# Optimization experiments

Hardware: AMD Instinct MI355X
Metric: run time of the kernel (lower is better)

The kernel has to match this reference:

```python
import jax, jax.numpy as jnp
import numpy as np

B, SQ, SC, DIM, H = 2, 2048, 2048, 1024, 16
HD = DIM // H  # 64
NEG = -10000.0


def setup_inputs() -> dict:
    key = jax.random.key(0)
    ks = jax.random.split(key, 12)
    x = jax.random.normal(ks[0], (B, SQ, DIM), dtype=jnp.float32)
    k_cache = jax.random.normal(ks[1], (B, SC, DIM), dtype=jnp.float32)
    v_cache = jax.random.normal(ks[2], (B, SC, DIM), dtype=jnp.float32)
    # binary additive-style mask (1 = masked), as multiplied by -10000 in forward
    mask = (jax.random.uniform(ks[3], (B, SQ, SQ + SC)) > 0.9).astype(jnp.float32)
    s = 1.0 / np.sqrt(DIM)
    Wq = jax.random.normal(ks[4], (DIM, DIM), dtype=jnp.float32) * s
    Wk = jax.random.normal(ks[5], (DIM, DIM), dtype=jnp.float32) * s
    Wv = jax.random.normal(ks[6], (DIM, DIM), dtype=jnp.float32) * s
    Wo = jax.random.normal(ks[7], (DIM, DIM), dtype=jnp.float32) * s
    bq = jnp.zeros((DIM,), jnp.float32)
    bk = jnp.zeros((DIM,), jnp.float32)
    bv = jnp.zeros((DIM,), jnp.float32)
    bo = jnp.zeros((DIM,), jnp.float32)
    return {"x": x, "k_cache": k_cache, "v_cache": v_cache, "mask": mask,
            "Wq": Wq, "bq": bq, "Wk": Wk, "bk": bk, "Wv": Wv, "bv": bv,
            "Wo": Wo, "bo": bo}


def reference(x, k_cache, v_cache, mask, Wq, bq, Wk, bk, Wv, bv, Wo, bo):
    # QKV projections (dropout is inference no-op)
    q = x @ Wq + bq                      # [B, SQ, DIM]
    k = jnp.concatenate([k_cache, x @ Wk + bk], axis=-2)  # [B, SKV, DIM]
    v = jnp.concatenate([v_cache, x @ Wv + bv], axis=-2)  # [B, SKV, DIM]
    skv = k.shape[-2]
    # split heads
    qh = q.reshape(B, SQ, H, HD).transpose(0, 2, 1, 3)    # [B, H, SQ, HD]
    kh = k.reshape(B, skv, H, HD).transpose(0, 2, 1, 3)   # [B, H, SKV, HD]
    vh = v.reshape(B, skv, H, HD).transpose(0, 2, 1, 3)   # [B, H, SKV, HD]
    scores = jnp.einsum('bhqd,bhkd->bhqk', qh, kh) / np.sqrt(HD)
    scores = scores + mask[:, None, :, :] * NEG           # additive mask
    attn = jax.nn.softmax(scores, axis=-1)
    ctx = jnp.einsum('bhqk,bhkd->bhqd', attn, vh)         # [B, H, SQ, HD]
    ctx = ctx.transpose(0, 2, 1, 3).reshape(B, SQ, DIM)
    out = ctx @ Wo + bo
    return (out, k, v)
```

## Files before the change

kernel.cpp:

```cpp
#include <hip/hip_runtime.h>
#include <hip/hip_bf16.h>

#define SQL  2048
#define SKVL 4096
#define DIML 1024

typedef __attribute__((ext_vector_type(8))) short short8;
typedef __attribute__((ext_vector_type(4))) float f32x4;

#define LOG2E 1.4426950408889634f
#define MBIGC (10000.0f * LOG2E)

#define GLL16(gptr, lptr)                                        \
  __builtin_amdgcn_global_load_lds(                              \
      (const __attribute__((address_space(1))) int*)(gptr),      \
      (__attribute__((address_space(3))) int*)(lptr), 16, 0, 0)

__device__ __forceinline__ short f2s(float f) {
  return __builtin_bit_cast(short, __float2bfloat16(f));
}
__device__ __forceinline__ float s2f(short s) {
  return __bfloat162float(__builtin_bit_cast(__hip_bfloat16, s));
}

__device__ __forceinline__ const char* swz_addr(const char* base, int row, int colByte) {
  return base + (row * 128 + (colByte ^ ((row & 7) << 4)));
}
__device__ __forceinline__ char* swz_addr(char* base, int row, int colByte) {
  return base + (row * 128 + (colByte ^ ((row & 7) << 4)));
}

__global__ __launch_bounds__(256) void prep_kernel(
    const float* __restrict__ x, short* __restrict__ xbf,
    const float* __restrict__ W0, const float* __restrict__ W1,
    const float* __restrict__ W2, const float* __restrict__ W3,
    short* __restrict__ WT,
    const float* __restrict__ kc, const float* __restrict__ vc,
    float* __restrict__ out, short* __restrict__ Kbf,
    const float* __restrict__ mask, unsigned long long* __restrict__ maskQ)
{
  __shared__ float T[64][65];
  const int bid = blockIdx.x;
  const int t = threadIdx.x;

  if (bid < 2048) {
    const size_t i = ((size_t)bid * 256 + t) * 8;
    float4 a = *(const float4*)&x[i];
    float4 b = *(const float4*)&x[i + 4];
    short8 o;
    o[0] = f2s(a.x); o[1] = f2s(a.y); o[2] = f2s(a.z); o[3] = f2s(a.w);
    o[4] = f2s(b.x); o[5] = f2s(b.y); o[6] = f2s(b.z); o[7] = f2s(b.w);
    *(short8*)&xbf[i] = o;
  } else if (bid < 3072) {
    const int lb = bid - 2048;
    const int w = lb >> 8;
    const float* W = (w == 0) ? W0 : (w == 1) ? W1 : (w == 2) ? W2 : W3;
    short* D = WT + (size_t)w * 1048576;
    const int tile = lb & 255;
    const int r0 = (tile >> 4) * 64;
    const int c0 = (tile & 15) * 64;
    const int row = t >> 2;
    const int q = t & 3;
#pragma unroll
    for (int i = 0; i < 4; i++)
      *(float4*)&T[row][q * 16 + i * 4] =
          *(const float4*)&W[(size_t)(r0 + row) * 1024 + c0 + q * 16 + i * 4];
    __syncthreads();
    short8 o0, o1;
#pragma unroll
    for (int j = 0; j < 8; j++) {
      o0[j] = f2s(T[q * 16 + j][row]);
      o1[j] = f2s(T[q * 16 + 8 + j][row]);
    }
    *(short8*)&D[(size_t)(c0 + row) * 1024 + r0 + q * 16] = o0;
    *(short8*)&D[(size_t)(c0 + row) * 1024 + r0 + q * 16 + 8] = o1;
  } else if (bid < 7168) {
    const int idx = (bid - 3072) * 256 + t;
    const int tensor = idx >> 19;
    const int cc = idx & 524287;
    const size_t e = (size_t)cc * 8;
    const int b = (int)(e >> 21);
    const size_t rem = e & 2097151;
    const float* src = tensor ? vc : kc;
    float* dst = out + (tensor ? 12582912u : 4194304u) + (size_t)b * 4194304u + rem;
    float4 a = *(const float4*)&src[e];
    float4 bb = *(const float4*)&src[e + 4];
    *(float4*)dst = a;
    *(float4*)(dst + 4) = bb;
    if (tensor == 0) {
      short8 o;
      o[0] = f2s(a.x); o[1] = f2s(a.y); o[2] = f2s(a.z); o[3] = f2s(a.w);
      o[4] = f2s(bb.x); o[5] = f2s(bb.y); o[6] = f2s(bb.z); o[7] = f2s(bb.w);
      *(short8*)&Kbf[(size_t)b * 4194304u + rem] = o;
    }
  } else {
    const int lb = bid - 7168;
    const int ktile = lb & 63;
    const int qtile = (lb >> 6) & 31;
    const int b = lb >> 11;
    const int q0 = qtile * 64, k0 = ktile * 64;
    const int row = t >> 2;
    const int q4 = t & 3;
    const float* src = mask + (size_t)(b * SQL + q0 + row) * SKVL + k0 + q4 * 16;
#pragma unroll
    for (int i = 0; i < 4; i++)
      *(float4*)&T[row][q4 * 16 + i * 4] = *(const float4*)&src[i * 4];
    __syncthreads();
    const int wv = t >> 6, ln = t & 63;
#pragma unroll
    for (int j = 0; j < 16; j++) {
      const int qrow = wv * 16 + j;
      unsigned long long w = __ballot(T[qrow][ln] > 0.5f);
      if (ln == 0)
        maskQ[(size_t)(b * SQL + q0 + qrow) * 64 + ktile] = w;
    }
  }
}

__global__ __launch_bounds__(256) void gemm_qkv(
    const short* __restrict__ A,
    const short* __restrict__ WT,
    const float* __restrict__ bq, const float* __restrict__ bk, const float* __restrict__ bv,
    short* __restrict__ qbf,
    float* __restrict__ kout, short* __restrict__ Kbf,
    float* __restrict__ vout, float qscale)
{
  constexpr int K = 1024;
  __shared__ __align__(16) short As[128 * 32];
  __shared__ __align__(16) short Bs[128 * 32];
  const int w = blockIdx.x >> 8;
  const int bid = blockIdx.x & 255;
  const int tid = threadIdx.x;
  const int lane = tid & 63;
  const int wave = tid >> 6;
  const int nb = bid & 7;
  const int mb = bid >> 3;
  const int wm = wave >> 1;
  const int wn = wave & 1;
  const int g = lane >> 4;
  const int fr = lane & 15;

  const short* BT = WT + (size_t)w * 1048576;
  const float* bias = (w == 0) ? bq : (w == 1) ? bk : bv;

  f32x4 acc[4][4] = {};

  const int c0 = tid, c1 = tid + 256;
  const short* Ab0 = A + (size_t)(mb * 128 + (c0 >> 2)) * K + (c0 & 3) * 8;
  const short* Ab1 = A + (size_t)(mb * 128 + (c1 >> 2)) * K + (c1 & 3) * 8;
  const short* Bb0 = BT + (size_t)(nb * 128 + (c0 >> 2)) * K + (c0 & 3) * 8;
  const short* Bb1 = BT + (size_t)(nb * 128 + (c1 >> 2)) * K + (c1 & 3) * 8;

  for (int k0 = 0; k0 < K; k0 += 32) {
    __syncthreads();
    GLL16(Ab0 + k0, &As[wave * 512]);
    GLL16(Ab1 + k0, &As[2048 + wave * 512]);
    GLL16(Bb0 + k0, &Bs[wave * 512]);
    GLL16(Bb1 + k0, &Bs[2048 + wave * 512]);
    __syncthreads();
    short8 af[4], bfv[4];
#pragma unroll
    for (int m = 0; m < 4; m++)
      af[m] = *(const short8*)&As[(wm * 64 + m * 16 + fr) * 32 + g * 8];
#pragma unroll
    for (int n = 0; n < 4; n++)
      bfv[n] = *(const short8*)&Bs[(wn * 64 + n * 16 + fr) * 32 + g * 8];
#pragma unroll
    for (int m = 0; m < 4; m++)
#pragma unroll
      for (int n = 0; n < 4; n++)
        acc[m][n] = __builtin_amdgcn_mfma_f32_16x16x32_bf16(af[m], bfv[n], acc[m][n], 0, 0, 0);
  }

  const int gm = mb * 128 + wm * 64;
  const int gn = nb * 128 + wn * 64;
  float bvv[4];
#pragma unroll
  for (int n = 0; n < 4; n++) bvv[n] = bias[gn + n * 16 + fr];
#pragma unroll
  for (int m = 0; m < 4; m++) {
#pragma unroll
    for (int r = 0; r < 4; r++) {
      const int row = gm + m * 16 + g * 4 + r;
      float vals[4];
      if (w == 0) {
#pragma unroll
        for (int n = 0; n < 4; n++) vals[n] = (acc[m][n][r] + bvv[n]) * qscale;
        const int drow = (row >> 11) * 2048 + (row & 2047);
#pragma unroll
        for (int n = 0; n < 4; n++)
          qbf[(size_t)drow * 1024 + gn + n * 16 + fr] = f2s(vals[n]);
      } else {
#pragma unroll
        for (int n = 0; n < 4; n++) vals[n] = acc[m][n][r] + bvv[n];
        const int drow = (row >> 11) * 4096 + 2048 + (row & 2047);
        if (w == 1) {
#pragma unroll
          for (int n = 0; n < 4; n++) {
            kout[(size_t)drow * 1024 + gn + n * 16 + fr] = vals[n];
            Kbf[(size_t)drow * 1024 + gn + n * 16 + fr] = f2s(vals[n]);
          }
        } else {
#pragma unroll
          for (int n = 0; n < 4; n++)
            vout[(size_t)drow * 1024 + gn + n * 16 + fr] = vals[n];
        }
      }
    }
  }
}

__global__ __launch_bounds__(256) void gemm_wo(
    const short* __restrict__ A,
    const short* __restrict__ BT,
    const float* __restrict__ bias,
    float* __restrict__ Cf)
{
  constexpr int K = 1024;
  __shared__ __align__(16) short As[128 * 32];
  __shared__ __align__(16) short Bs[64 * 32];
  const int tid = threadIdx.x;
  const int lane = tid & 63;
  const int wave = tid >> 6;
  const int bid = blockIdx.x;
  const int nb = bid & 15;
  const int mb = bid >> 4;
  const int wm = wave >> 1;
  const int wn = wave & 1;
  const int g = lane >> 4;
  const int fr = lane & 15;

  f32x4 acc[4][2] = {};

  const int c0 = tid, c1 = tid + 256;
  const short* Ab0 = A + (size_t)(mb * 128 + (c0 >> 2)) * K + (c0 & 3) * 8;
  const short* Ab1 = A + (size_t)(mb * 128 + (c1 >> 2)) * K + (c1 & 3) * 8;
  const short* Bb0 = BT + (size_t)(nb * 64 + (c0 >> 2)) * K + (c0 & 3) * 8;

  for (int k0 = 0; k0 < K; k0 += 32) {
    __syncthreads();
    GLL16(Ab0 + k0, &As[wave * 512]);
    GLL16(Ab1 + k0, &As[2048 + wave * 512]);
    GLL16(Bb0 + k0, &Bs[wave * 512]);
    __syncthreads();
    short8 af[4], bfv[2];
#pragma unroll
    for (int m = 0; m < 4; m++)
      af[m] = *(const short8*)&As[(wm * 64 + m * 16 + fr) * 32 + g * 8];
#pragma unroll
    for (int n = 0; n < 2; n++)
      bfv[n] = *(const short8*)&Bs[(wn * 32 + n * 16 + fr) * 32 + g * 8];
#pragma unroll
    for (int m = 0; m < 4; m++)
#pragma unroll
      for (int n = 0; n < 2; n++)
        acc[m][n] = __builtin_amdgcn_mfma_f32_16x16x32_bf16(af[m], bfv[n], acc[m][n], 0, 0, 0);
  }

  const int gm = mb * 128 + wm * 64;
  const int gn = nb * 64 + wn * 32;
  float bv[2];
#pragma unroll
  for (int n = 0; n < 2; n++) bv[n] = bias[gn + n * 16 + fr];
#pragma unroll
  for (int m = 0; m < 4; m++) {
#pragma unroll
    for (int r = 0; r < 4; r++) {
      const int row = gm + m * 16 + g * 4 + r;
#pragma unroll
      for (int n = 0; n < 2; n++)
        Cf[(size_t)row * 1024 + gn + n * 16 + fr] = acc[m][n][r] + bv[n];
    }
  }
}

__global__ __launch_bounds__(256) void transpose_v_kernel(
    const float* __restrict__ Vf, short* __restrict__ VT)
{
  __shared__ float T[64][65];
  const int bid = blockIdx.x;
  const int kb = bid & 63;
  const int h = (bid >> 6) & 15;
  const int b = bid >> 10;
  const int kt = kb * 64;
  const int t = threadIdx.x;
  const int row = t >> 2;
  const int q = t & 3;
  const float* src = Vf + (size_t)(b * SKVL + kt + row) * DIML + h * 64 + q * 16;
#pragma unroll
  for (int i = 0; i < 4; i++)
    *(float4*)&T[row][q * 16 + i * 4] = *(const float4*)&src[i * 4];
  __syncthreads();
  short8 o0, o1;
#pragma unroll
  for (int j = 0; j < 8; j++) {
    o0[j] = f2s(T[q * 16 + j][row]);
    o1[j] = f2s(T[q * 16 + 8 + j][row]);
  }
  short* D = VT + (size_t)((b * 16 + h) * 64 + row) * SKVL + kt;
  *(short8*)&D[q * 16] = o0;
  *(short8*)&D[q * 16 + 8] = o1;
}

__global__ __launch_bounds__(512) void attn_kernel(
    const short* __restrict__ Q,
    const short* __restrict__ Kb_,
    const short* __restrict__ VT_,
    const unsigned long long* __restrict__ maskQ,
    short* __restrict__ pctx,
    float2* __restrict__ ml)
{
  __shared__ __align__(16) char LDSB[32768];
  const int tid = threadIdx.x;
  const int lane = tid & 63;
  const int wave = tid >> 6;
  const int gid = blockIdx.x;
  const int xcd = gid & 7;
  const int seq = gid >> 3;
  const int group = xcd * 8 + (seq >> 4);
  const int qbB = seq & 15;
  const int half = group & 1;
  const int bh = group >> 1;
  const int b = bh >> 4;
  const int h = bh & 15;
  const int g = lane >> 4;
  const int c = lane & 15;

  const int qbase = qbB * 128 + wave * 16;

  short8 qf[2];
  {
    const short* qp = Q + (size_t)(b * SQL + qbase + c) * DIML + h * 64 + g * 8;
    qf[0] = *(const short8*)qp;
    qf[1] = *(const short8*)(qp + 32);
  }

  short8 vone;
#pragma unroll
  for (int j = 0; j < 8; j++) vone[j] = (short)0x3F80;

  float m_run = -1e30f;
  f32x4 ctx[4] = {};
  f32x4 lacc = {};

  const unsigned X = (unsigned)((c & 7) << 4);
  unsigned kA  = (unsigned)(c * 128) + (((unsigned)(g * 16)) ^ X);
  unsigned vA  = 8192u + (unsigned)(c * 128) + (((unsigned)(g * 16)) ^ X);
  unsigned pw0 = 16384u + (unsigned)(wave * 2048 + c * 128) +
                 (((unsigned)(g * 8)) ^ (X & 0x10u)) + (X & 0x60u);
  unsigned pr0 = 16384u + (unsigned)(wave * 2048 + c * 128) +
                 (((unsigned)(g * 16)) ^ X);
  asm volatile("" : "+v"(kA), "+v"(vA), "+v"(pw0), "+v"(pr0));

  const int k_beg = half * (SKVL / 2);
  const int srow = lane >> 3;
  const int scol = ((lane & 7) ^ srow) * 8;
  const short* gk = Kb_ + (size_t)b * SKVL * DIML + h * 64 +
                    (size_t)(k_beg + wave * 8 + srow) * DIML + scol;
  const short* gv = VT_ + (size_t)(b * 16 + h) * 64 * SKVL +
                    (size_t)(wave * 8 + srow) * SKVL + k_beg + scol;
  const unsigned long long* mqp =
      maskQ + (size_t)(b * SQL + qbase + c) * 64 + half * 32;
  const unsigned kdst = (unsigned)(wave * 8 * 128);
  const unsigned vdst = 8192u + (unsigned)(wave * 8 * 128);

  for (int t = 0; t < (SKVL / 2) / 64; t++) {
    if (t) __syncthreads();
    GLL16(gk, &LDSB[kdst]);
    GLL16(gv, &LDSB[vdst]);
    gk += 64 * DIML;
    gv += 64;
    const unsigned long long mq = *mqp++;

    __syncthreads();

    f32x4 s[4] = {};
#pragma unroll
    for (int n = 0; n < 4; n++) {
      short8 kf0 = *(const short8*)&LDSB[kA + (unsigned)(n * 2048)];
      short8 kf1 = *(const short8*)&LDSB[(kA ^ 64u) + (unsigned)(n * 2048)];
      s[n] = __builtin_amdgcn_mfma_f32_16x16x32_bf16(kf0, qf[0], s[n], 0, 0, 0);
      s[n] = __builtin_amdgcn_mfma_f32_16x16x32_bf16(kf1, qf[1], s[n], 0, 0, 0);
    }
#pragma unroll
    for (int n = 0; n < 4; n++) {
      const unsigned wn = (unsigned)(mq >> (n * 16 + g * 4)) & 0xFu;
#pragma unroll
      for (int r = 0; r < 4; r++)
        if ((wn >> r) & 1u) s[n][r] -= MBIGC;
    }
    float mx0 = fmaxf(fmaxf(s[0][0], s[0][1]), fmaxf(s[0][2], s[0][3]));
    float mx1 = fmaxf(fmaxf(s[1][0], s[1][1]), fmaxf(s[1][2], s[1][3]));
    float mx2 = fmaxf(fmaxf(s[2][0], s[2][1]), fmaxf(s[2][2], s[2][3]));
    float mx3 = fmaxf(fmaxf(s[3][0], s[3][1]), fmaxf(s[3][2], s[3][3]));
    const float mloc = fmaxf(fmaxf(mx0, mx1), fmaxf(mx2, mx3));
    if (__any(mloc > m_run + 11.5f)) {
      float mt = fmaxf(mloc, __shfl_xor(mloc, 16));
      mt = fmaxf(mt, __shfl_xor(mt, 32));
      const float mnew = fmaxf(m_run, mt);
      const float sc = exp2f(m_run - mnew);
      m_run = mnew;
#pragma unroll
      for (int r = 0; r < 4; r++) {
        const float scr = __shfl(sc, g * 4 + r);
        lacc[r] *= scr;
        ctx[0][r] *= scr; ctx[1][r] *= scr; ctx[2][r] *= scr; ctx[3][r] *= scr;
      }
    }
#pragma unroll
    for (int n = 0; n < 4; n++) {
      const float p0 = exp2f(s[n][0] - m_run);
      const float p1 = exp2f(s[n][1] - m_run);
      const float p2 = exp2f(s[n][2] - m_run);
      const float p3 = exp2f(s[n][3] - m_run);
      unsigned lo, hi;
      asm("v_cvt_pk_bf16_f32 %0, %1, %2" : "=v"(lo) : "v"(p0), "v"(p1));
      asm("v_cvt_pk_bf16_f32 %0, %1, %2" : "=v"(hi) : "v"(p2), "v"(p3));
      *(uint2*)&LDSB[pw0 ^ (unsigned)(n * 32)] = make_uint2(lo, hi);
    }
#pragma unroll
    for (int ks = 0; ks < 2; ks++) {
      short8 pa = *(const short8*)&LDSB[pr0 ^ (unsigned)(ks * 64)];
      lacc = __builtin_amdgcn_mfma_f32_16x16x32_bf16(pa, vone, lacc, 0, 0, 0);
#pragma unroll
      for (int d = 0; d < 4; d++) {
        short8 vfr = *(const short8*)&LDSB[(vA ^ (unsigned)(ks * 64)) + (unsigned)(d * 2048)];
        ctx[d] = __builtin_amdgcn_mfma_f32_16x16x32_bf16(pa, vfr, ctx[d], 0, 0, 0);
      }
    }
  }

#pragma unroll
  for (int r = 0; r < 4; r++) {
    const int rg = ((b * 16 + h) << 11) + qbase + g * 4 + r;
    const size_t base = ((size_t)half << 22) + (size_t)rg * 64;
#pragma unroll
    for (int d = 0; d < 4; d++)
      pctx[base + d * 16 + c] = f2s(ctx[d][r]);
    const float m_q = __shfl(m_run, g * 4 + r);
    if (c == 0) ml[half * 65536 + rg] = make_float2(m_q, lacc[r]);
  }
}

__global__ __launch_bounds__(256) void combine_kernel(
    const short* __restrict__ pctx, const float2* __restrict__ ml,
    short* __restrict__ ctxb)
{
  const int t = blockIdx.x * 256 + threadIdx.x;
  const int r = t >> 2;
  const int seg = (t & 3) * 16;
  const float2 ml0 = ml[r];
  const float2 ml1 = ml[65536 + r];
  const float m = fmaxf(ml0.x, ml1.x);
  const float w0 = exp2f(ml0.x - m);
  const float w1 = exp2f(ml1.x - m);
  const float inv = 1.0f / (ml0.y * w0 + ml1.y * w1);
  const short8 a0 = *(const short8*)&pctx[(size_t)r * 64 + seg];
  const short8 a1 = *(const short8*)&pctx[(size_t)r * 64 + seg + 8];
  const short8 b0 = *(const short8*)&pctx[(1ull << 22) + (size_t)r * 64 + seg];
  const short8 b1 = *(const short8*)&pctx[(1ull << 22) + (size_t)r * 64 + seg + 8];
  short8 o0, o1;
#pragma unroll
  for (int j = 0; j < 8; j++) {
    o0[j] = f2s((s2f(a0[j]) * w0 + s2f(b0[j]) * w1) * inv);
    o1[j] = f2s((s2f(a1[j]) * w0 + s2f(b1[j]) * w1) * inv);
  }
  const int b = r >> 15;
  const int h = (r >> 11) & 15;
  const int q = r & 2047;
  short* D = ctxb + (size_t)(b * 2048 + q) * 1024 + h * 64 + seg;
  *(short8*)&D[0] = o0;
  *(short8*)&D[8] = o1;
}

extern "C" void kernel_launch(void* const* d_in, const int* in_sizes, int n_in,
                              void* d_out, int out_size, void* d_ws, size_t ws_size,
                              hipStream_t stream)
{
  const float* x   = (const float*)d_in[0];
  const float* kc  = (const float*)d_in[1];
  const float* vc  = (const float*)d_in[2];
  const float* msk = (const float*)d_in[3];
  const float* Wq  = (const float*)d_in[4];
  const float* bq  = (const float*)d_in[5];
  const float* Wk  = (const float*)d_in[6];
  const float* bk  = (const float*)d_in[7];
  const float* Wv  = (const float*)d_in[8];
  const float* bv  = (const float*)d_in[9];
  const float* Wo  = (const float*)d_in[10];
  const float* bo  = (const float*)d_in[11];

  float* outf = (float*)d_out;
  float* kout = outf + 4194304;
  float* vout = outf + 12582912;

  short* ws_s  = (short*)d_ws;
  short* WT    = ws_s;
  short* xbf   = ws_s + (size_t)4 * 1048576;
  short* qbf   = ws_s + (size_t)8 * 1048576;
  short* Kbf   = ws_s + (size_t)12 * 1048576;
  short* VTb   = ws_s + (size_t)20 * 1048576;
  unsigned long long* maskQ = (unsigned long long*)(ws_s + (size_t)28 * 1048576);
  short* pctx  = ws_s + (size_t)44 * 1048576;
  float2* mlp  = (float2*)(ws_s + (size_t)52 * 1048576);
  short* ctxb  = xbf;

  const float qscale = 0.125f * LOG2E;

  prep_kernel<<<11264, 256, 0, stream>>>(x, xbf, Wq, Wk, Wv, Wo, WT,
                                         kc, vc, outf, Kbf, msk, maskQ);
  gemm_qkv<<<768, 256, 0, stream>>>(xbf, WT, bq, bk, bv, qbf, kout, Kbf, vout, qscale);
  transpose_v_kernel<<<2048, 256, 0, stream>>>(vout, VTb);
  attn_kernel<<<1024, 512, 0, stream>>>(qbf, Kbf, VTb, maskQ, pctx, mlp);
  combine_kernel<<<1024, 256, 0, stream>>>(pctx, mlp, ctxb);
  gemm_wo<<<512, 256, 0, stream>>>(ctxb, WT + 3 * 1048576, bo, outf);
}
```

Measured before the change: 256.3 us.

## Double-buffer K tiles in LDS and apply mask as zeroing after exp

The attention loop now double-buffers K tiles in LDS. The next K tile and the current V tile are issued before the QK MFMAs, and the barriers move so the V load overlaps QK and softmax work. The mask is no longer subtracted from the scores before the max; masked probabilities are set to zero after exp2, which drops a dependent step before the row max. In exchange, LDS grows to 40 KB per block. The final iteration prefetches a K tile past the half's range, and the running max can now include masked scores.

```diff
diff --git a/kernel.cpp b/kernel.cpp
--- a/kernel.cpp
+++ b/kernel.cpp
@@ -9,7 +9,6 @@
 typedef __attribute__((ext_vector_type(4))) float f32x4;
 
 #define LOG2E 1.4426950408889634f
-#define MBIGC (10000.0f * LOG2E)
 
 #define GLL16(gptr, lptr)                                        \
   __builtin_amdgcn_global_load_lds(                              \
@@ -21,13 +20,6 @@
 }
 __device__ __forceinline__ float s2f(short s) {
   return __bfloat162float(__builtin_bit_cast(__hip_bfloat16, s));
-}
-
-__device__ __forceinline__ const char* swz_addr(const char* base, int row, int colByte) {
-  return base + (row * 128 + (colByte ^ ((row & 7) << 4)));
-}
-__device__ __forceinline__ char* swz_addr(char* base, int row, int colByte) {
-  return base + (row * 128 + (colByte ^ ((row & 7) << 4)));
 }
 
 __global__ __launch_bounds__(256) void prep_kernel(
@@ -310,7 +302,7 @@
     short* __restrict__ pctx,
     float2* __restrict__ ml)
 {
-  __shared__ __align__(16) char LDSB[32768];
+  __shared__ __align__(16) char LDSB[40960];
   const int tid = threadIdx.x;
   const int lane = tid & 63;
   const int wave = tid >> 6;
@@ -345,10 +337,10 @@
 
   const unsigned X = (unsigned)((c & 7) << 4);
   unsigned kA  = (unsigned)(c * 128) + (((unsigned)(g * 16)) ^ X);
-  unsigned vA  = 8192u + (unsigned)(c * 128) + (((unsigned)(g * 16)) ^ X);
-  unsigned pw0 = 16384u + (unsigned)(wave * 2048 + c * 128) +
+  unsigned vA  = 16384u + (unsigned)(c * 128) + (((unsigned)(g * 16)) ^ X);
+  unsigned pw0 = 24576u + (unsigned)(wave * 2048 + c * 128) +
                  (((unsigned)(g * 8)) ^ (X & 0x10u)) + (X & 0x60u);
-  unsigned pr0 = 16384u + (unsigned)(wave * 2048 + c * 128) +
+  unsigned pr0 = 24576u + (unsigned)(wave * 2048 + c * 128) +
                  (((unsigned)(g * 16)) ^ X);
   asm volatile("" : "+v"(kA), "+v"(vA), "+v"(pw0), "+v"(pr0));
 
@@ -361,33 +353,27 @@
                     (size_t)(wave * 8 + srow) * SKVL + k_beg + scol;
   const unsigned long long* mqp =
       maskQ + (size_t)(b * SQL + qbase + c) * 64 + half * 32;
-  const unsigned kdst = (unsigned)(wave * 8 * 128);
-  const unsigned vdst = 8192u + (unsigned)(wave * 8 * 128);
+  const unsigned wdst = (unsigned)(wave * 1024);
+
+  GLL16(gk, &LDSB[wdst]);
+  gk += 64 * DIML;
+  __syncthreads();
+  unsigned kcur = 0;
 
   for (int t = 0; t < (SKVL / 2) / 64; t++) {
-    if (t) __syncthreads();
-    GLL16(gk, &LDSB[kdst]);
-    GLL16(gv, &LDSB[vdst]);
+    GLL16(gv, &LDSB[16384u + wdst]);
+    gv += 64;
+    GLL16(gk, &LDSB[(kcur ^ 8192u) + wdst]);
     gk += 64 * DIML;
-    gv += 64;
     const unsigned long long mq = *mqp++;
 
-    __syncthreads();
-
     f32x4 s[4] = {};
 #pragma unroll
     for (int n = 0; n < 4; n++) {
-      short8 kf0 = *(const short8*)&LDSB[kA + (unsigned)(n * 2048)];
-      short8 kf1 = *(const short8*)&LDSB[(kA ^ 64u) + (unsigned)(n * 2048)];
+      short8 kf0 = *(const short8*)&LDSB[kcur + kA + (unsigned)(n * 2048)];
+      short8 kf1 = *(const short8*)&LDSB[kcur + (kA ^ 64u) + (unsigned)(n * 2048)];
       s[n] = __builtin_amdgcn_mfma_f32_16x16x32_bf16(kf0, qf[0], s[n], 0, 0, 0);
       s[n] = __builtin_amdgcn_mfma_f32_16x16x32_bf16(kf1, qf[1], s[n], 0, 0, 0);
-    }
-#pragma unroll
-    for (int n = 0; n < 4; n++) {
-      const unsigned wn = (unsigned)(mq >> (n * 16 + g * 4)) & 0xFu;
-#pragma unroll
-      for (int r = 0; r < 4; r++)
-        if ((wn >> r) & 1u) s[n][r] -= MBIGC;
     }
     float mx0 = fmaxf(fmaxf(s[0][0], s[0][1]), fmaxf(s[0][2], s[0][3]));
     float mx1 = fmaxf(fmaxf(s[1][0], s[1][1]), fmaxf(s[1][2], s[1][3]));
@@ -409,15 +395,23 @@
     }
 #pragma unroll
     for (int n = 0; n < 4; n++) {
-      const float p0 = exp2f(s[n][0] - m_run);
-      const float p1 = exp2f(s[n][1] - m_run);
-      const float p2 = exp2f(s[n][2] - m_run);
-      const float p3 = exp2f(s[n][3] - m_run);
+      const unsigned wn = (unsigned)(mq >> (n * 16 + g * 4)) & 0xFu;
+      float p0 = exp2f(s[n][0] - m_run);
+      float p1 = exp2f(s[n][1] - m_run);
+      float p2 = exp2f(s[n][2] - m_run);
+      float p3 = exp2f(s[n][3] - m_run);
+      p0 = (wn & 1u) ? 0.0f : p0;
+      p1 = (wn & 2u) ? 0.0f : p1;
+      p2 = (wn & 4u) ? 0.0f : p2;
+      p3 = (wn & 8u) ? 0.0f : p3;
       unsigned lo, hi;
       asm("v_cvt_pk_bf16_f32 %0, %1, %2" : "=v"(lo) : "v"(p0), "v"(p1));
       asm("v_cvt_pk_bf16_f32 %0, %1, %2" : "=v"(hi) : "v"(p2), "v"(p3));
       *(uint2*)&LDSB[pw0 ^ (unsigned)(n * 32)] = make_uint2(lo, hi);
     }
+
+    __syncthreads();
+
 #pragma unroll
     for (int ks = 0; ks < 2; ks++) {
       short8 pa = *(const short8*)&LDSB[pr0 ^ (unsigned)(ks * 64)];
@@ -428,6 +422,9 @@
         ctx[d] = __builtin_amdgcn_mfma_f32_16x16x32_bf16(pa, vfr, ctx[d], 0, 0, 0);
       }
     }
+
+    __syncthreads();
+    kcur ^= 8192u;
   }
 
 #pragma unroll
```

Measured after the change: 253.5 us. Within noise of the previous version (-1.1%).
